# Optimization experiments

Measured on AMD Instinct MI355X. Metric: run time of the kernel, lower is better.

The kernel has to match this reference:

```python
import jax, jax.numpy as jnp
import numpy as np

NUM_HEADS = 16
SOFTPLUS_EPS = 1e-4


def rotate_half(x):
    x1, x2 = jnp.split(x, 2, axis=-1)
    return jnp.concatenate((-x2, x1), axis=-1)


def setup_inputs() -> dict:
    key = jax.random.key(0)
    B, S, H = 1, 2048, 2048
    D = H // NUM_HEADS  # 128
    ks = jax.random.split(key, 5)
    hidden_states = jax.random.normal(ks[0], (B, S, H), dtype=jnp.float32)
    # standard RoPE tables: [S, D]
    inv_freq = 1.0 / (10000.0 ** (np.arange(0, D, 2, dtype=np.float32) / D))
    freqs = np.outer(np.arange(S, dtype=np.float32), inv_freq)  # [S, D/2]
    emb = np.concatenate([freqs, freqs], axis=-1)  # [S, D]
    cos = jnp.asarray(np.cos(emb), dtype=jnp.float32)
    sin = jnp.asarray(np.sin(emb), dtype=jnp.float32)
    std = 0.02
    w_q = jax.random.normal(ks[1], (2 * H, H), dtype=jnp.float32) * std
    w_k = jax.random.normal(ks[2], (2 * H, H), dtype=jnp.float32) * std
    w_v = jax.random.normal(ks[3], (H, H), dtype=jnp.float32) * std
    w_o = jax.random.normal(ks[4], (H, H), dtype=jnp.float32) * std
    return {"hidden_states": hidden_states, "cos": cos, "sin": sin,
            "w_q": w_q, "w_k": w_k, "w_v": w_v, "w_o": w_o}


def reference(hidden_states, cos, sin, w_q, w_k, w_v, w_o):
    B, S, H = hidden_states.shape
    NH = NUM_HEADS
    D = H // NH
    # projections (torch Linear: y = x @ W.T)
    q = (hidden_states @ w_q.T).reshape(B, S, NH, 2 * D).swapaxes(1, 2)  # [B,NH,S,2D]
    k = (hidden_states @ w_k.T).reshape(B, S, NH, 2 * D).swapaxes(1, 2)
    v = (hidden_states @ w_v.T).reshape(B, S, NH, D).swapaxes(1, 2)      # [B,NH,S,D]
    q_mu, q_sigma_raw = jnp.split(q, 2, axis=-1)
    k_mu, k_sigma_raw = jnp.split(k, 2, axis=-1)
    q_sigma = jax.nn.softplus(q_sigma_raw) + SOFTPLUS_EPS
    k_sigma = jax.nn.softplus(k_sigma_raw) + SOFTPLUS_EPS
    q_w = q_mu / jnp.sqrt(q_sigma)
    k_w = k_mu / jnp.sqrt(k_sigma)
    # RoPE on variance-weighted means; cos/sin [S,D] broadcast over [B,NH,S,D]
    q_w = q_w * cos + rotate_half(q_w) * sin
    k_w = k_w * cos + rotate_half(k_w) * sin
    q_sq = jnp.sum(q_w * q_w, axis=-1, keepdims=True)          # [B,NH,S,1]
    k_sq = jnp.sum(k_w * k_w, axis=-1, keepdims=True)          # [B,NH,S,1]
    dot = jnp.einsum('bhqd,bhkd->bhqk', q_w, k_w)              # [B,NH,S,S]
    weighted_dist = q_sq + jnp.swapaxes(k_sq, -2, -1) - 2.0 * dot
    log_det_q = jnp.sum(jnp.log(q_sigma), axis=-1, keepdims=True)
    log_det_k = jnp.sum(jnp.log(k_sigma), axis=-1, keepdims=True)
    log_det = log_det_q + jnp.swapaxes(log_det_k, -2, -1)
    attn_scores = -0.5 * (weighted_dist + log_det)
    attn_probs = jax.nn.softmax(attn_scores, axis=-1)
    attn_out = jnp.einsum('bhqk,bhkd->bhqd', attn_probs, v)    # [B,NH,S,D]
    attn_out = attn_out.swapaxes(1, 2).reshape(B, S, H)
    return attn_out @ w_o.T
```

## Files before the change

kernel.cpp:

```cpp
#include <hip/hip_runtime.h>
#include <stdint.h>

#define S_LEN 2048
#define HID   2048
#define NHEAD 16
#define HD    128
#define NQK   8192
#define K_HID 2048

typedef _Float16 f16x8 __attribute__((ext_vector_type(8)));
typedef float    f32x4 __attribute__((ext_vector_type(4)));

__device__ __forceinline__ unsigned short f2h(float f) {
    _Float16 h = (_Float16)f;
    union { _Float16 h; unsigned short u; } c; c.h = h;
    return c.u;
}
__device__ __forceinline__ float h2f(unsigned short b) {
    union { unsigned short u; _Float16 h; } c; c.u = b;
    return (float)c.h;
}
__device__ __forceinline__ float softplus_f(float x) {
    return (x > 20.f) ? x : log1pf(expf(x));
}
__device__ __forceinline__ void gload_lds16(const unsigned short* g, unsigned short* l) {
    __builtin_amdgcn_global_load_lds(
        (const __attribute__((address_space(1))) unsigned int*)g,
        (__attribute__((address_space(3))) unsigned int*)l, 16, 0, 0);
}

__global__ __launch_bounds__(256) void cast5(const float* __restrict__ hs,
                                             const float* __restrict__ wq,
                                             const float* __restrict__ wk,
                                             const float* __restrict__ wv,
                                             const float* __restrict__ wo,
                                             unsigned short* __restrict__ hs16,
                                             unsigned short* __restrict__ wqk16,
                                             unsigned short* __restrict__ wv16,
                                             unsigned short* __restrict__ wo16) {
    int b = blockIdx.x;
    const float* src;
    unsigned short* dst;
    int i;
    if (b < 4096)       { src = hs; dst = hs16;                          i = b; }
    else if (b < 12288) { src = wq; dst = wqk16;                         i = b - 4096; }
    else if (b < 20480) { src = wk; dst = wqk16 + (size_t)4096 * K_HID;  i = b - 12288; }
    else if (b < 24576) { src = wv; dst = wv16;                          i = b - 20480; }
    else                { src = wo; dst = wo16;                          i = b - 24576; }
    int idx = i * 256 + threadIdx.x;
    float4 v = ((const float4*)src)[idx];
    ushort4 o;
    o.x = f2h(v.x); o.y = f2h(v.y); o.z = f2h(v.z); o.w = f2h(v.w);
    ((ushort4*)dst)[idx] = o;
}

template <bool OUT_F16>
__global__ __launch_bounds__(256) void gemm_nt_f16(const unsigned short* __restrict__ A,
                                                   const unsigned short* __restrict__ B,
                                                   void* __restrict__ Cv,
                                                   int M, int N, int Kd) {
    __shared__ __align__(16) unsigned short As[128 * 32];
    __shared__ __align__(16) unsigned short Bs[128 * 32];
    const int t    = threadIdx.x;
    const int m0   = blockIdx.y * 128;
    const int n0   = blockIdx.x * 128;
    const int wave = t >> 6;
    const int lane = t & 63;
    const int wm   = wave >> 1, wn = wave & 1;
    const int lrow = lane & 15, quad = lane >> 4;
    const int srow = lane >> 2;
    const int scol = (lane & 3) * 8;

    f32x4 acc[4][4];
    for (int i = 0; i < 4; ++i)
        for (int j = 0; j < 4; ++j)
            acc[i][j] = (f32x4){0.f, 0.f, 0.f, 0.f};

    for (int k0 = 0; k0 < Kd; k0 += 32) {
        for (int c = 0; c < 2; ++c) {
            int ch = wave * 2 + c;
            int row = ch * 16 + srow;
            gload_lds16(A + (size_t)(m0 + row) * Kd + k0 + scol, &As[ch * 512]);
            gload_lds16(B + (size_t)(n0 + row) * Kd + k0 + scol, &Bs[ch * 512]);
        }
        __syncthreads();

        f16x8 af[4], bfr[4];
        for (int tm = 0; tm < 4; ++tm)
            af[tm]  = *(const f16x8*)(&As[(wm * 64 + tm * 16 + lrow) * 32 + quad * 8]);
        for (int tn = 0; tn < 4; ++tn)
            bfr[tn] = *(const f16x8*)(&Bs[(wn * 64 + tn * 16 + lrow) * 32 + quad * 8]);
        for (int tm = 0; tm < 4; ++tm)
            for (int tn = 0; tn < 4; ++tn)
                acc[tm][tn] = __builtin_amdgcn_mfma_f32_16x16x32_f16(af[tm], bfr[tn], acc[tm][tn], 0, 0, 0);
        __syncthreads();
    }

    for (int tm = 0; tm < 4; ++tm)
        for (int tn = 0; tn < 4; ++tn) {
            int col = n0 + wn * 64 + tn * 16 + lrow;
            for (int r = 0; r < 4; ++r) {
                int row = m0 + wm * 64 + tm * 16 + quad * 4 + r;
                if (OUT_F16)
                    ((unsigned short*)Cv)[(size_t)row * N + col] = f2h(acc[tm][tn][r]);
                else
                    ((float*)Cv)[(size_t)row * N + col] = acc[tm][tn][r];
            }
        }
}

__global__ __launch_bounds__(256) void prep_qk(const float* __restrict__ qk,
                                               const float* __restrict__ cosb,
                                               const float* __restrict__ sinb,
                                               unsigned short* __restrict__ Q16,
                                               unsigned short* __restrict__ K16,
                                               float* __restrict__ kbias) {
    int gid  = blockIdx.x * 4 + (threadIdx.x >> 6);
    int lane = threadIdx.x & 63;
    int h = gid >> 11;
    int s = gid & 2047;
    int d1 = lane, d2 = lane + 64;
    const float* row = qk + (size_t)s * NQK;
    float c1 = cosb[s * HD + d1], c2 = cosb[s * HD + d2];
    float s1 = sinb[s * HD + d1], s2 = sinb[s * HD + d2];
    size_t ob = ((size_t)h * S_LEN + s) * HD;

    {
        int base = h * 256;
        float mu1 = row[base + d1],            mu2 = row[base + d2];
        float sg1 = softplus_f(row[base + 128 + d1]) + 1e-4f;
        float sg2 = softplus_f(row[base + 128 + d2]) + 1e-4f;
        float w1 = mu1 * rsqrtf(sg1), w2 = mu2 * rsqrtf(sg2);
        float o1 = w1 * c1 - w2 * s1;
        float o2 = w2 * c2 + w1 * s2;
        Q16[ob + d1] = f2h(o1);
        Q16[ob + d2] = f2h(o2);
    }
    {
        int base = 4096 + h * 256;
        float mu1 = row[base + d1],            mu2 = row[base + d2];
        float sg1 = softplus_f(row[base + 128 + d1]) + 1e-4f;
        float sg2 = softplus_f(row[base + 128 + d2]) + 1e-4f;
        float w1 = mu1 * rsqrtf(sg1), w2 = mu2 * rsqrtf(sg2);
        float o1 = w1 * c1 - w2 * s1;
        float o2 = w2 * c2 + w1 * s2;
        unsigned short k1 = f2h(o1), k2 = f2h(o2);
        K16[ob + d1] = k1; K16[ob + d2] = k2;
        float r1 = h2f(k1), r2 = h2f(k2);
        float part = r1 * r1 + r2 * r2 + logf(sg1) + logf(sg2);
        for (int off = 32; off > 0; off >>= 1) part += __shfl_down(part, off);
        if (lane == 0) kbias[(size_t)h * S_LEN + s] = -0.5f * part;
    }
}

__global__ __launch_bounds__(256, 2) void flash_mfma(const unsigned short* __restrict__ Q16,
                                                     const unsigned short* __restrict__ K16,
                                                     const unsigned short* __restrict__ Vt,
                                                     const float* __restrict__ kbias,
                                                     float* __restrict__ OP,
                                                     float* __restrict__ ML) {
    constexpr int LV = 72;
    __shared__ __align__(16) unsigned short Khs[4 * 64 * 32];
    __shared__ __align__(16) unsigned short Vts[2 * 128 * 32];
    __shared__ __align__(16) unsigned short Ps[128 * LV];
    __shared__ float kb[64];

    const int t    = threadIdx.x;
    const int h    = blockIdx.y;
    const int q0   = blockIdx.x * 128;
    const int kz   = blockIdx.z;
    const int wave = t >> 6;
    const int lane = t & 63;
    const int lrow = lane & 15, quad = lane >> 4;
    const int srow = lane >> 2;
    const int scol = (lane & 3) * 8;

    f16x8 qf[2][4];
    for (int m = 0; m < 2; ++m) {
        size_t rb = ((size_t)h * S_LEN + q0 + wave * 32 + m * 16 + lrow) * HD;
        for (int kk = 0; kk < 4; ++kk)
            qf[m][kk] = *(const f16x8*)(Q16 + rb + kk * 32 + quad * 8);
    }

    float mrow[2][4], lsum[2][4];
    f32x4 Ofr[2][8];
    for (int m = 0; m < 2; ++m)
        for (int r = 0; r < 4; ++r) { mrow[m][r] = -INFINITY; lsum[m][r] = 0.f; }
    for (int m = 0; m < 2; ++m)
        for (int d = 0; d < 8; ++d) Ofr[m][d] = (f32x4){0.f, 0.f, 0.f, 0.f};

    const int kbeg = kz * 1024;
    for (int k0 = kbeg; k0 < kbeg + 1024; k0 += 64) {
        {
            const unsigned short* kgb = K16 + ((size_t)h * S_LEN + k0) * HD;
            const unsigned short* vgb = Vt + ((size_t)h * HD) * S_LEN + k0;
            for (int c = 0; c < 4; ++c) {
                int ch = wave * 4 + c;
                int kk = ch >> 2;
                int r  = (ch & 3) * 16 + srow;
                gload_lds16(kgb + (size_t)r * HD + kk * 32 + scol, &Khs[ch * 512]);
                int kc = ch >> 3;
                int r2 = (ch & 7) * 16 + srow;
                gload_lds16(vgb + (size_t)r2 * S_LEN + kc * 32 + scol, &Vts[ch * 512]);
            }
            if (t < 64) kb[t] = kbias[(size_t)h * S_LEN + k0 + t];
        }
        __syncthreads();

        f32x4 sc[2][4];
        for (int m = 0; m < 2; ++m)
            for (int nt = 0; nt < 4; ++nt) sc[m][nt] = (f32x4){0.f, 0.f, 0.f, 0.f};
        for (int kk = 0; kk < 4; ++kk)
            for (int nt = 0; nt < 4; ++nt) {
                f16x8 khf = *(const f16x8*)(&Khs[kk * 2048 + (nt * 16 + lrow) * 32 + quad * 8]);
                sc[0][nt] = __builtin_amdgcn_mfma_f32_16x16x32_f16(qf[0][kk], khf, sc[0][nt], 0, 0, 0);
                sc[1][nt] = __builtin_amdgcn_mfma_f32_16x16x32_f16(qf[1][kk], khf, sc[1][nt], 0, 0, 0);
            }
        float kbn[4] = {kb[lrow], kb[16 + lrow], kb[32 + lrow], kb[48 + lrow]};

        for (int m = 0; m < 2; ++m)
            for (int r = 0; r < 4; ++r) {
                float s0 = sc[m][0][r] + kbn[0];
                float s1 = sc[m][1][r] + kbn[1];
                float s2 = sc[m][2][r] + kbn[2];
                float s3 = sc[m][3][r] + kbn[3];
                float mx = fmaxf(fmaxf(s0, s1), fmaxf(s2, s3));
                mx = fmaxf(mx, __shfl_xor(mx, 1));
                mx = fmaxf(mx, __shfl_xor(mx, 2));
                mx = fmaxf(mx, __shfl_xor(mx, 4));
                mx = fmaxf(mx, __shfl_xor(mx, 8));
                float mnew  = fmaxf(mrow[m][r], mx);
                float alpha = __expf(mrow[m][r] - mnew);
                mrow[m][r] = mnew;
                float p0 = __expf(s0 - mnew);
                float p1 = __expf(s1 - mnew);
                float p2 = __expf(s2 - mnew);
                float p3 = __expf(s3 - mnew);
                lsum[m][r] = lsum[m][r] * alpha + ((p0 + p1) + (p2 + p3));
                for (int d = 0; d < 8; ++d) Ofr[m][d][r] *= alpha;
                int prow = (wave * 32 + m * 16 + quad * 4 + r) * LV;
                Ps[prow + lrow]      = f2h(p0);
                Ps[prow + 16 + lrow] = f2h(p1);
                Ps[prow + 32 + lrow] = f2h(p2);
                Ps[prow + 48 + lrow] = f2h(p3);
            }

        for (int c = 0; c < 2; ++c) {
            f16x8 pa0 = *(const f16x8*)(&Ps[(wave * 32 + lrow) * LV + c * 32 + quad * 8]);
            f16x8 pa1 = *(const f16x8*)(&Ps[(wave * 32 + 16 + lrow) * LV + c * 32 + quad * 8]);
            for (int dt = 0; dt < 8; ++dt) {
                f16x8 vb = *(const f16x8*)(&Vts[c * 4096 + (dt * 16 + lrow) * 32 + quad * 8]);
                Ofr[0][dt] = __builtin_amdgcn_mfma_f32_16x16x32_f16(pa0, vb, Ofr[0][dt], 0, 0, 0);
                Ofr[1][dt] = __builtin_amdgcn_mfma_f32_16x16x32_f16(pa1, vb, Ofr[1][dt], 0, 0, 0);
            }
        }
        __syncthreads();
    }

    size_t obase = (size_t)(kz * NHEAD + h) * S_LEN;
    for (int m = 0; m < 2; ++m)
        for (int r = 0; r < 4; ++r) {
            float rs = lsum[m][r];
            rs += __shfl_xor(rs, 1);
            rs += __shfl_xor(rs, 2);
            rs += __shfl_xor(rs, 4);
            rs += __shfl_xor(rs, 8);
            int qrow = q0 + wave * 32 + m * 16 + quad * 4 + r;
            float* op = OP + (obase + qrow) * HD;
            for (int dt = 0; dt < 8; ++dt)
                op[dt * 16 + lrow] = Ofr[m][dt][r];
            if (lrow == 0) {
                ML[(obase + qrow) * 2]     = mrow[m][r];
                ML[(obase + qrow) * 2 + 1] = rs;
            }
        }
}

__global__ __launch_bounds__(256) void flash_merge(const float* __restrict__ OP,
                                                   const float* __restrict__ ML,
                                                   unsigned short* __restrict__ Obf) {
    int row = blockIdx.x * 2 + (threadIdx.x >> 7);
    int d   = threadIdx.x & 127;
    int h = row >> 11, q = row & 2047;
    size_t i0 = (size_t)h * S_LEN + q;
    size_t i1 = (size_t)(NHEAD + h) * S_LEN + q;
    float m0 = ML[i0 * 2], l0 = ML[i0 * 2 + 1];
    float m1 = ML[i1 * 2], l1 = ML[i1 * 2 + 1];
    float mf = fmaxf(m0, m1);
    float w0 = __expf(m0 - mf), w1 = __expf(m1 - mf);
    float inv = 1.f / (l0 * w0 + l1 * w1);
    float o = (OP[i0 * HD + d] * w0 + OP[i1 * HD + d] * w1) * inv;
    Obf[(size_t)q * HID + h * HD + d] = f2h(o);
}

extern "C" void kernel_launch(void* const* d_in, const int* in_sizes, int n_in,
                              void* d_out, int out_size, void* d_ws, size_t ws_size,
                              hipStream_t stream) {
    const float* hs   = (const float*)d_in[0];
    const float* cosb = (const float*)d_in[1];
    const float* sinb = (const float*)d_in[2];
    const float* wq   = (const float*)d_in[3];
    const float* wk   = (const float*)d_in[4];
    const float* wv   = (const float*)d_in[5];
    const float* wo   = (const float*)d_in[6];
    float* out = (float*)d_out;
    char*  ws  = (char*)d_ws;

    unsigned short* w_qk16 = (unsigned short*)(ws);
    unsigned short* Q16    = (unsigned short*)(ws);
    unsigned short* K16    = (unsigned short*)(ws + 8388608);
    float*          kbias  = (float*)(ws + 16777216);
    float*          qk_f32 = (float*)(ws + 33554432);
    float*          OP     = (float*)(ws + 33554432);
    float*          ML     = (float*)(ws + 33554432 + 33554432);
    unsigned short* hs16   = (unsigned short*)(ws + 100663296);
    unsigned short* Obf    = (unsigned short*)(ws + 100663296);
    unsigned short* w_v16  = (unsigned short*)(ws + 109051904);
    unsigned short* w_o16  = (unsigned short*)(ws + 117440512);
    unsigned short* Vt     = (unsigned short*)(ws + 125829120);

    cast5<<<28672, 256, 0, stream>>>(hs, wq, wk, wv, wo, hs16, w_qk16, w_v16, w_o16);

    gemm_nt_f16<false><<<dim3(64, 16), 256, 0, stream>>>(hs16, w_qk16, qk_f32,
                                                         S_LEN, NQK, K_HID);
    gemm_nt_f16<true><<<dim3(16, 16), 256, 0, stream>>>(w_v16, hs16, Vt, HID, S_LEN, K_HID);
    prep_qk<<<(NHEAD * S_LEN) / 4, 256, 0, stream>>>(qk_f32, cosb, sinb,
                                                     Q16, K16, kbias);
    flash_mfma<<<dim3(S_LEN / 128, NHEAD, 2), 256, 0, stream>>>(Q16, K16, Vt,
                                                                kbias, OP, ML);
    flash_merge<<<(NHEAD * S_LEN) / 2, 256, 0, stream>>>(OP, ML, Obf);
    gemm_nt_f16<false><<<dim3(16, 16), 256, 0, stream>>>(Obf, w_o16, out, S_LEN, HID, K_HID);
}
```

Baseline: 443.5 us.

## Merge QK and V projection GEMMs into one launch with fp16 intermediates

```diff
diff --git a/kernel.cpp b/kernel.cpp
--- a/kernel.cpp
+++ b/kernel.cpp
@@ -55,15 +55,12 @@
 }
 
 template <bool OUT_F16>
-__global__ __launch_bounds__(256) void gemm_nt_f16(const unsigned short* __restrict__ A,
-                                                   const unsigned short* __restrict__ B,
-                                                   void* __restrict__ Cv,
-                                                   int M, int N, int Kd) {
-    __shared__ __align__(16) unsigned short As[128 * 32];
-    __shared__ __align__(16) unsigned short Bs[128 * 32];
+__device__ __forceinline__ void gemm_body(const unsigned short* __restrict__ A,
+                                          const unsigned short* __restrict__ B,
+                                          void* __restrict__ Cv,
+                                          int m0, int n0, int N,
+                                          unsigned short* As, unsigned short* Bs) {
     const int t    = threadIdx.x;
-    const int m0   = blockIdx.y * 128;
-    const int n0   = blockIdx.x * 128;
     const int wave = t >> 6;
     const int lane = t & 63;
     const int wm   = wave >> 1, wn = wave & 1;
@@ -76,12 +73,12 @@
         for (int j = 0; j < 4; ++j)
             acc[i][j] = (f32x4){0.f, 0.f, 0.f, 0.f};
 
-    for (int k0 = 0; k0 < Kd; k0 += 32) {
+    for (int k0 = 0; k0 < K_HID; k0 += 32) {
         for (int c = 0; c < 2; ++c) {
             int ch = wave * 2 + c;
             int row = ch * 16 + srow;
-            gload_lds16(A + (size_t)(m0 + row) * Kd + k0 + scol, &As[ch * 512]);
-            gload_lds16(B + (size_t)(n0 + row) * Kd + k0 + scol, &Bs[ch * 512]);
+            gload_lds16(A + (size_t)(m0 + row) * K_HID + k0 + scol, &As[ch * 512]);
+            gload_lds16(B + (size_t)(n0 + row) * K_HID + k0 + scol, &Bs[ch * 512]);
         }
         __syncthreads();
 
@@ -109,7 +106,33 @@
         }
 }
 
-__global__ __launch_bounds__(256) void prep_qk(const float* __restrict__ qk,
+__global__ __launch_bounds__(256) void gemm_qkv(const unsigned short* __restrict__ hs16,
+                                                const unsigned short* __restrict__ wqk16,
+                                                const unsigned short* __restrict__ wv16,
+                                                unsigned short* __restrict__ qk16,
+                                                unsigned short* __restrict__ Vt) {
+    __shared__ __align__(16) unsigned short As[128 * 32];
+    __shared__ __align__(16) unsigned short Bs[128 * 32];
+    int b = blockIdx.x;
+    if (b < 1024) {
+        gemm_body<true>(hs16, wqk16, qk16, (b >> 6) * 128, (b & 63) * 128, NQK, As, Bs);
+    } else {
+        b -= 1024;
+        gemm_body<true>(wv16, hs16, Vt, (b >> 4) * 128, (b & 15) * 128, S_LEN, As, Bs);
+    }
+}
+
+template <bool OUT_F16>
+__global__ __launch_bounds__(256) void gemm_nt_f16(const unsigned short* __restrict__ A,
+                                                   const unsigned short* __restrict__ B,
+                                                   void* __restrict__ Cv,
+                                                   int M, int N, int Kd) {
+    __shared__ __align__(16) unsigned short As[128 * 32];
+    __shared__ __align__(16) unsigned short Bs[128 * 32];
+    gemm_body<OUT_F16>(A, B, Cv, blockIdx.y * 128, blockIdx.x * 128, N, As, Bs);
+}
+
+__global__ __launch_bounds__(256) void prep_qk(const unsigned short* __restrict__ qk,
                                                const float* __restrict__ cosb,
                                                const float* __restrict__ sinb,
                                                unsigned short* __restrict__ Q16,
@@ -120,16 +143,16 @@
     int h = gid >> 11;
     int s = gid & 2047;
     int d1 = lane, d2 = lane + 64;
-    const float* row = qk + (size_t)s * NQK;
+    const unsigned short* row = qk + (size_t)s * NQK;
     float c1 = cosb[s * HD + d1], c2 = cosb[s * HD + d2];
     float s1 = sinb[s * HD + d1], s2 = sinb[s * HD + d2];
     size_t ob = ((size_t)h * S_LEN + s) * HD;
 
     {
         int base = h * 256;
-        float mu1 = row[base + d1],            mu2 = row[base + d2];
-        float sg1 = softplus_f(row[base + 128 + d1]) + 1e-4f;
-        float sg2 = softplus_f(row[base + 128 + d2]) + 1e-4f;
+        float mu1 = h2f(row[base + d1]),       mu2 = h2f(row[base + d2]);
+        float sg1 = softplus_f(h2f(row[base + 128 + d1])) + 1e-4f;
+        float sg2 = softplus_f(h2f(row[base + 128 + d2])) + 1e-4f;
         float w1 = mu1 * rsqrtf(sg1), w2 = mu2 * rsqrtf(sg2);
         float o1 = w1 * c1 - w2 * s1;
         float o2 = w2 * c2 + w1 * s2;
@@ -138,9 +161,9 @@
     }
     {
         int base = 4096 + h * 256;
-        float mu1 = row[base + d1],            mu2 = row[base + d2];
-        float sg1 = softplus_f(row[base + 128 + d1]) + 1e-4f;
-        float sg2 = softplus_f(row[base + 128 + d2]) + 1e-4f;
+        float mu1 = h2f(row[base + d1]),       mu2 = h2f(row[base + d2]);
+        float sg1 = softplus_f(h2f(row[base + 128 + d1])) + 1e-4f;
+        float sg2 = softplus_f(h2f(row[base + 128 + d2])) + 1e-4f;
         float w1 = mu1 * rsqrtf(sg1), w2 = mu2 * rsqrtf(sg2);
         float o1 = w1 * c1 - w2 * s1;
         float o2 = w2 * c2 + w1 * s2;
@@ -157,7 +180,7 @@
                                                      const unsigned short* __restrict__ K16,
                                                      const unsigned short* __restrict__ Vt,
                                                      const float* __restrict__ kbias,
-                                                     float* __restrict__ OP,
+                                                     unsigned short* __restrict__ OP,
                                                      float* __restrict__ ML) {
     constexpr int LV = 72;
     __shared__ __align__(16) unsigned short Khs[4 * 64 * 32];
@@ -266,9 +289,9 @@
             rs += __shfl_xor(rs, 4);
             rs += __shfl_xor(rs, 8);
             int qrow = q0 + wave * 32 + m * 16 + quad * 4 + r;
-            float* op = OP + (obase + qrow) * HD;
+            unsigned short* op = OP + (obase + qrow) * HD;
             for (int dt = 0; dt < 8; ++dt)
-                op[dt * 16 + lrow] = Ofr[m][dt][r];
+                op[dt * 16 + lrow] = f2h(Ofr[m][dt][r]);
             if (lrow == 0) {
                 ML[(obase + qrow) * 2]     = mrow[m][r];
                 ML[(obase + qrow) * 2 + 1] = rs;
@@ -276,7 +299,7 @@
         }
 }
 
-__global__ __launch_bounds__(256) void flash_merge(const float* __restrict__ OP,
+__global__ __launch_bounds__(256) void flash_merge(const unsigned short* __restrict__ OP,
                                                    const float* __restrict__ ML,
                                                    unsigned short* __restrict__ Obf) {
     int row = blockIdx.x * 2 + (threadIdx.x >> 7);
@@ -289,7 +312,7 @@
     float mf = fmaxf(m0, m1);
     float w0 = __expf(m0 - mf), w1 = __expf(m1 - mf);
     float inv = 1.f / (l0 * w0 + l1 * w1);
-    float o = (OP[i0 * HD + d] * w0 + OP[i1 * HD + d] * w1) * inv;
+    float o = (h2f(OP[i0 * HD + d]) * w0 + h2f(OP[i1 * HD + d]) * w1) * inv;
     Obf[(size_t)q * HID + h * HD + d] = f2h(o);
 }
 
@@ -310,21 +333,20 @@
     unsigned short* Q16    = (unsigned short*)(ws);
     unsigned short* K16    = (unsigned short*)(ws + 8388608);
     float*          kbias  = (float*)(ws + 16777216);
-    float*          qk_f32 = (float*)(ws + 33554432);
-    float*          OP     = (float*)(ws + 33554432);
-    float*          ML     = (float*)(ws + 33554432 + 33554432);
-    unsigned short* hs16   = (unsigned short*)(ws + 100663296);
-    unsigned short* Obf    = (unsigned short*)(ws + 100663296);
-    unsigned short* w_v16  = (unsigned short*)(ws + 109051904);
-    unsigned short* w_o16  = (unsigned short*)(ws + 117440512);
-    unsigned short* Vt     = (unsigned short*)(ws + 125829120);
+    unsigned short* qk16   = (unsigned short*)(ws + 33554432);
+    unsigned short* OP     = (unsigned short*)(ws + 33554432);
+    float*          ML     = (float*)(ws + 50331648);
+    unsigned short* hs16   = (unsigned short*)(ws + 67108864);
+    unsigned short* Obf    = (unsigned short*)(ws + 67108864);
+    unsigned short* w_v16  = (unsigned short*)(ws + 75497472);
+    unsigned short* w_o16  = (unsigned short*)(ws + 83886080);
+    unsigned short* Vt     = (unsigned short*)(ws + 92274688);
 
     cast5<<<28672, 256, 0, stream>>>(hs, wq, wk, wv, wo, hs16, w_qk16, w_v16, w_o16);
 
-    gemm_nt_f16<false><<<dim3(64, 16), 256, 0, stream>>>(hs16, w_qk16, qk_f32,
-                                                         S_LEN, NQK, K_HID);
-    gemm_nt_f16<true><<<dim3(16, 16), 256, 0, stream>>>(w_v16, hs16, Vt, HID, S_LEN, K_HID);
-    prep_qk<<<(NHEAD * S_LEN) / 4, 256, 0, stream>>>(qk_f32, cosb, sinb,
+    gemm_qkv<<<1280, 256, 0, stream>>>(hs16, w_qk16, w_v16, qk16, Vt);
+
+    prep_qk<<<(NHEAD * S_LEN) / 4, 256, 0, stream>>>(qk16, cosb, sinb,
                                                      Q16, K16, kbias);
     flash_mfma<<<dim3(S_LEN / 128, NHEAD, 2), 256, 0, stream>>>(Q16, K16, Vt,
                                                                 kbias, OP, ML);
```

Result: faster. 398.3 us (-10.2%).
